# Optimization experiments

Hardware: AMD Instinct MI355X
Metric: run time of the kernel (lower is better)

Reference implementation:

```python
import jax, jax.numpy as jnp
import numpy as np

INFTY_APPROX = 1e30
LAM = 10000.0


def sinusoid_embs(length, width):
    # Transformer-XL sinusoidal embeddings, flipped so row 0 encodes the
    # largest relative distance (length-1), matching the rel_shift convention.
    pos = jnp.arange(length, dtype=jnp.float32)
    inv_lams = 1.0 / (LAM ** (jnp.arange(0, width, 2, dtype=jnp.float32) / width))
    pre = pos[:, None] * inv_lams[None, :]                 # [T, width//2]
    cat = jnp.concatenate([jnp.sin(pre), jnp.cos(pre)], axis=-1)  # [T, width]
    return jnp.flip(cat, axis=0)


def rel_shift(x):
    # x: [B, T, T] -> out[b,i,j] = x[b, i, j - i + T - 1] (XL pad/reshape trick)
    b, t, _ = x.shape
    x = jnp.pad(x, ((0, 0), (0, 0), (1, 0)))               # [B, T, T+1]
    x = x.reshape(b, t + 1, t)[:, 1:, :]                   # [B, T, T]
    return x


def setup_inputs() -> dict:
    B, T, D, K, V = 2, 4096, 1024, 128, 2048
    key = jax.random.key(0)
    ks = jax.random.split(key, 10)
    s_d = 1.0 / np.sqrt(D)
    s_v = 1.0 / np.sqrt(V)
    return {
        'x':    jax.random.normal(ks[0], (B, T, D), dtype=jnp.float32),
        'g_ln': jnp.ones((D,), dtype=jnp.float32),
        'W_q':  s_d * jax.random.normal(ks[1], (D, K), dtype=jnp.float32),
        'W_k':  s_d * jax.random.normal(ks[2], (D, K), dtype=jnp.float32),
        'W_v':  s_d * jax.random.normal(ks[3], (D, V), dtype=jnp.float32),
        'W_g':  s_d * jax.random.normal(ks[4], (D, V), dtype=jnp.float32),
        'W_r':  s_d * jax.random.normal(ks[5], (D, K), dtype=jnp.float32),
        'xl_u': 0.02 * jax.random.normal(ks[6], (K,), dtype=jnp.float32),
        'xl_v': 0.02 * jax.random.normal(ks[7], (K,), dtype=jnp.float32),
        'W_o':  s_v * jax.random.normal(ks[8], (V, D), dtype=jnp.float32),
    }


def reference(x, g_ln, W_q, W_k, W_v, W_g, W_r, xl_u, xl_v, W_o):
    B, T, D = x.shape
    K = W_q.shape[-1]
    tau = jnp.asarray(K, x.dtype) ** 0.5

    # RMSNorm input layernorm
    x_tilde = x * jax.lax.rsqrt(jnp.mean(jnp.square(x), axis=-1, keepdims=True) + 1e-6)
    x_tilde = x_tilde * g_ln

    # QKVG projections; queries pre-scaled by 1/tau (producer-side scaling)
    q = (x_tilde @ W_q) / tau                              # [B, T, K]
    k = x_tilde @ W_k                                      # [B, T, K]
    v = x_tilde @ W_v                                      # [B, T, V]

    # XL relative-position bias inputs
    xl_r = sinusoid_embs(T, D) @ W_r                       # [T, K]

    # AC term (content) and BD term (position) with XL u/v biases
    scores_ac = jnp.einsum('bik,bjk->bij', q + xl_u, k)    # [B, T, T]
    scores_bd = jnp.einsum('bik,jk->bij', q + xl_v, xl_r)  # [B, T, T]
    scores_bd = rel_shift(scores_bd)

    scores = scores_ac + scores_bd
    keep = jnp.tril(jnp.ones((T, T), dtype=bool))          # causal keep mask
    scores = scores - jnp.asarray(INFTY_APPROX, x.dtype) * jnp.logical_not(keep)

    w = jax.nn.softmax(scores, axis=-1)                    # [B, T, T]
    wv = jnp.einsum('bij,bjv->biv', w, v)                  # [B, T, V]

    # SHGA gating (GAU-style silu gate)
    wv = wv * jax.nn.silu(x_tilde @ W_g)

    res = wv @ W_o                                         # [B, T, D]
    return res
```

## Files before the change

kernel.cpp:

```cpp
#include <hip/hip_runtime.h>
#include <hip/hip_bf16.h>
#include <stdint.h>

typedef __attribute__((ext_vector_type(4))) float f32x4;
typedef __attribute__((ext_vector_type(8))) short s16x8;
typedef __attribute__((ext_vector_type(8))) unsigned short u16x8;
typedef __attribute__((ext_vector_type(4))) unsigned short u16x4;

static __device__ __forceinline__ float b2f(unsigned short u) {
  union { unsigned int i; float f; } v; v.i = ((unsigned int)u) << 16; return v.f;
}
static __device__ __forceinline__ unsigned short f2b(float f) {
  unsigned int x = __float_as_uint(f);
  return (unsigned short)((x + 0x7fffu + ((x >> 16) & 1u)) >> 16);
}

typedef __attribute__((address_space(1))) const void gconst_t;
typedef __attribute__((address_space(3))) void lds_t;
static __device__ __forceinline__ void gload_lds16(const void* g, void* l) {
  __builtin_amdgcn_global_load_lds((gconst_t*)g, (lds_t*)l, 16, 0, 0);
}

template<int N>
static __device__ __forceinline__ void vmwait() {
  asm volatile("s_waitcnt vmcnt(%0)" :: "n"(N) : "memory");
}
static __device__ __forceinline__ void barmid() {
  __builtin_amdgcn_sched_barrier(0);
  __builtin_amdgcn_s_barrier();
  asm volatile("s_waitcnt lgkmcnt(0)" ::: "memory");
  __builtin_amdgcn_sched_barrier(0);
}
static __device__ __forceinline__ void barend() {
  __builtin_amdgcn_sched_barrier(0);
  __builtin_amdgcn_s_barrier();
}

struct GemmP {
  const unsigned short* A; const unsigned short* B; void* C;
  long sA, sB, sC;
  int M, N, K, lda, ldb, ldc;
  int causal, kend_mode, swapxy;
  int gxs, gys, qchunk;
  const float* uvec; const float* vvec;
  unsigned short* qv_out; unsigned short* kk_out; float invtau;
  const float* rinv; const unsigned short* gate;
  const unsigned short* bds; float* stats;
};

template<int EPI>
__launch_bounds__(512, 2)
__global__ void gemm8p256_k(GemmP p) {
  __shared__ unsigned short L[2][4][8192];
  const int lin = (int)blockIdx.x + (int)gridDim.x * ((int)blockIdx.y + (int)gridDim.y * (int)blockIdx.z);
  const int wg = (lin & 7) * p.qchunk + (lin >> 3);
  const int xx = wg & ((1 << p.gxs) - 1);
  const int yy = (wg >> p.gxs) & ((1 << p.gys) - 1);
  const int ii = p.swapxy ? yy : xx;
  const int jj = p.swapxy ? xx : yy;
  const int i0 = ii * 256, j0 = jj * 256;
  const unsigned short* Ag = p.A + (long)i0 * p.lda;
  const unsigned short* Bg = p.B + (long)j0 * p.ldb;
  const int lda = p.lda, ldb = p.ldb;
  const int NI = p.K >> 7;

  const int tid = threadIdx.x;
  const int w = tid >> 6, l = tid & 63;
  const int wr = w >> 2, wc = w & 3;
  const int fr = l & 15, fq = l >> 4;

  auto stA = [&](int slot, int h, int t) {
#pragma unroll
    for (int u = 0; u < 2; ++u) {
      const int sl = u * 512 + tid, r = sl >> 3, g = sl & 7;
      const int gs = g ^ (r & 7);
      gload_lds16(Ag + (long)(h * 128 + r) * lda + t * 64 + gs * 8, &L[slot][h][sl * 8]);
    }
  };
  auto stB = [&](int slot, int h, int t) {
#pragma unroll
    for (int u = 0; u < 2; ++u) {
      const int sl = u * 512 + tid, r = sl >> 3, g = sl & 7;
      const int gs = g ^ (r & 7);
      gload_lds16(Bg + (long)(h * 128 + r) * ldb + t * 64 + gs * 8, &L[slot][2 + h][sl * 8]);
    }
  };

  f32x4 acc[8][4];
#pragma unroll
  for (int m = 0; m < 8; ++m)
#pragma unroll
    for (int n = 0; n < 4; ++n) acc[m][n] = (f32x4){0.f, 0.f, 0.f, 0.f};

  const int sx = (fr & 7) << 4;
  const int abase = ((fr << 7) + (fq << 4)) ^ sx;
  const int bbase = (((wc & 1) << 13) + (fr << 7) + (fq << 4)) ^ sx;
  s16x8 a[4][2], bA[2][2], bB[2][2];

  auto rdA = [&](int slot, int mq) {
#pragma unroll
    for (int m = 0; m < 4; ++m)
#pragma unroll
      for (int ks = 0; ks < 2; ++ks)
        a[m][ks] = *(const s16x8*)((const char*)&L[slot][wr][0] +
                                   ((abase ^ (ks << 6)) | ((mq * 4 + m) << 11)));
  };
  auto rdB = [&](int slot, int nq, s16x8 (&bb)[2][2]) {
    const int reg = 2 + (wc >> 1);
#pragma unroll
    for (int n = 0; n < 2; ++n)
#pragma unroll
      for (int ks = 0; ks < 2; ++ks)
        bb[n][ks] = *(const s16x8*)((const char*)&L[slot][reg][0] +
                                    ((bbase ^ (ks << 6)) | ((nq * 2 + n) << 11)));
  };
  auto mm = [&](int mq, int nq, s16x8 (&bb)[2][2]) {
    __builtin_amdgcn_s_setprio(1);
#pragma unroll
    for (int m = 0; m < 4; ++m)
#pragma unroll
      for (int n = 0; n < 2; ++n)
#pragma unroll
        for (int ks = 0; ks < 2; ++ks)
          acc[mq * 4 + m][nq * 2 + n] =
              __builtin_amdgcn_mfma_f32_16x16x32_bf16(a[m][ks], bb[n][ks],
                                                      acc[mq * 4 + m][nq * 2 + n], 0, 0, 0);
    __builtin_amdgcn_s_setprio(0);
  };

  stB(0, 0, 0); stB(0, 1, 0); stA(0, 0, 0); stA(0, 1, 0);
  stB(1, 0, 1); stB(1, 1, 1);
  vmwait<4>();
  barend();

  for (int it = 0; it < NI; ++it) {
    const int t0 = 2 * it, t1 = t0 + 1;
    const bool lastI = (it == NI - 1);
    rdA(0, 0); rdB(0, 0, bA); stA(1, 0, t1);
    barmid(); mm(0, 0, bA); barend();
    rdB(0, 1, bB); stA(1, 1, t1);
    barmid(); mm(0, 1, bB); barend();
    rdA(0, 1);
    if (!lastI) stB(0, 0, t0 + 2);
    barmid(); mm(1, 1, bB); barend();
    if (!lastI) stB(0, 1, t0 + 2);
    barmid(); mm(1, 0, bA);
    if (lastI) vmwait<0>(); else vmwait<4>();
    barend();
    rdA(1, 0); rdB(1, 0, bA);
    if (!lastI) stA(0, 0, t0 + 2);
    barmid(); mm(0, 0, bA); barend();
    rdB(1, 1, bB);
    if (!lastI) stA(0, 1, t0 + 2);
    barmid(); mm(0, 1, bB); barend();
    rdA(1, 1);
    if (!lastI) stB(1, 0, t1 + 2);
    barmid(); mm(1, 1, bB); barend();
    if (!lastI) stB(1, 1, t1 + 2);
    barmid(); mm(1, 0, bA);
    if (!lastI) vmwait<4>();
    barend();
  }

  const int rb = i0 + wr * 128 + fq * 4;
  const int cb = j0 + wc * 64 + fr;
#pragma unroll
  for (int m = 0; m < 8; ++m)
#pragma unroll
    for (int n = 0; n < 4; ++n) {
      const int col = cb + n * 16;
#pragma unroll
      for (int e = 0; e < 4; ++e) {
        const int row = rb + m * 16 + e;
        const float val = acc[m][n][e];
        if constexpr (EPI == 0)
          ((unsigned short*)p.C)[(long)row * p.ldc + col] = f2b(val);
        else
          ((unsigned short*)p.C)[(long)row * p.ldc + col] = f2b(val / (1.f + __expf(-val)));
      }
    }
}

template<int PAIR, int EPI>
__launch_bounds__(512, 2)
__global__ void gemm8p128_k(GemmP p) {
  __shared__ unsigned short L[3][3][8192];
  const int lin = (int)blockIdx.x + (int)gridDim.x * ((int)blockIdx.y + (int)gridDim.y * (int)blockIdx.z);
  const int wg = (lin & 7) * p.qchunk + (lin >> 3);
  const int xx = wg & ((1 << p.gxs) - 1);
  const int yy = (wg >> p.gxs) & ((1 << p.gys) - 1);
  const int b  = wg >> (p.gxs + p.gys);
  const int jj = PAIR ? yy : (p.swapxy ? xx : yy);
  const int j0 = jj * 128;
  const unsigned short* Bg0 = p.B + (long)b * p.sB + (long)j0 * p.ldb;
  const int lda = p.lda, ldb = p.ldb;

  const int tid = threadIdx.x;
  const int w = tid >> 6, l = tid & 63;
  const int wr = w >> 1, wc = w & 1;
  const int fr = l & 15, fq = l >> 4;

  const int sx = (fr & 7) << 4;
  const int abase = ((((wr & 1) << 13) + (fr << 7) + (fq << 4))) ^ sx;
  const int bbase = (((wc << 13) + (fr << 7) + (fq << 4))) ^ sx;

  const int passes = PAIR ? 2 : 1;
  for (int ps = 0; ps < passes; ++ps) {
    const int ii = PAIR ? (ps ? xx : (15 - xx)) : (p.swapxy ? yy : xx);
    const int i0 = ii * 256;
    const unsigned short* Ag = p.A + (long)b * p.sA + (long)i0 * lda;
    const int kend = p.kend_mode ? min(p.K, i0 + 256) : p.K;
    const int NT = kend >> 6;

    auto stA = [&](int slot, int h, int t) {
#pragma unroll
      for (int u = 0; u < 2; ++u) {
        const int sl = u * 512 + tid, r = sl >> 3, g = sl & 7;
        const int gs = g ^ (r & 7);
        gload_lds16(Ag + (long)(h * 128 + r) * lda + t * 64 + gs * 8, &L[slot][h][sl * 8]);
      }
    };
    auto stB = [&](int slot, int bh, int t) {
      const int r = tid >> 3, g = tid & 7;
      const int rloc = bh * 64 + r;
      const int gs = g ^ (rloc & 7);
      gload_lds16(Bg0 + (long)rloc * ldb + t * 64 + gs * 8, &L[slot][2][bh * 4096 + tid * 8]);
    };

    f32x4 acc[4][4];
#pragma unroll
    for (int m = 0; m < 4; ++m)
#pragma unroll
      for (int n = 0; n < 4; ++n) acc[m][n] = (f32x4){0.f, 0.f, 0.f, 0.f};
    s16x8 a[4][2], bA[2][2], bB[2][2];

    auto rdA = [&](int slot) {
      const int reg = wr >> 1;
#pragma unroll
      for (int m = 0; m < 4; ++m)
#pragma unroll
        for (int ks = 0; ks < 2; ++ks)
          a[m][ks] = *(const s16x8*)((const char*)&L[slot][reg][0] +
                                     ((abase ^ (ks << 6)) | (m << 11)));
    };
    auto rdB = [&](int slot, int nq, s16x8 (&bb)[2][2]) {
#pragma unroll
      for (int n = 0; n < 2; ++n)
#pragma unroll
        for (int ks = 0; ks < 2; ++ks)
          bb[n][ks] = *(const s16x8*)((const char*)&L[slot][2][0] +
                                      ((bbase ^ (ks << 6)) | ((nq * 2 + n) << 11)));
    };
    auto mm = [&](int nq, s16x8 (&bb)[2][2]) {
      __builtin_amdgcn_s_setprio(1);
#pragma unroll
      for (int m = 0; m < 4; ++m)
#pragma unroll
        for (int n = 0; n < 2; ++n)
#pragma unroll
          for (int ks = 0; ks < 2; ++ks)
            acc[m][nq * 2 + n] =
                __builtin_amdgcn_mfma_f32_16x16x32_bf16(a[m][ks], bb[n][ks],
                                                        acc[m][nq * 2 + n], 0, 0, 0);
      __builtin_amdgcn_s_setprio(0);
    };

    stA(0, 0, 0); stB(0, 0, 0); stA(0, 1, 0); stB(0, 1, 0);
    stA(1, 0, 1); stB(1, 0, 1); stA(1, 1, 1); stB(1, 1, 1);
    vmwait<6>();
    barend();

    int s = 0;
    for (int t = 0; t < NT; ++t) {
      int s2 = s + 2; if (s2 >= 3) s2 -= 3;
      const bool pf = (t + 2 < NT);
      rdA(s); rdB(s, 0, bA);
      if (pf) { stA(s2, 0, t + 2); stB(s2, 0, t + 2); }
      barmid(); mm(0, bA); barend();
      rdB(s, 1, bB);
      if (pf) { stA(s2, 1, t + 2); stB(s2, 1, t + 2); }
      barmid(); mm(1, bB);
      if (t == NT - 2) vmwait<0>(); else if (t < NT - 2) vmwait<6>();
      barend();
      s = (s + 1 == 3) ? 0 : s + 1;
    }

    const int rb = i0 + wr * 64 + fq * 4;
    const int cb = j0 + wc * 64 + fr;
    const long tb = (long)b * p.sC;
#pragma unroll
    for (int m = 0; m < 4; ++m)
#pragma unroll
      for (int n = 0; n < 4; ++n) {
        const int col = cb + n * 16;
#pragma unroll
        for (int e = 0; e < 4; ++e) {
          const int row = rb + m * 16 + e;
          const float val = acc[m][n][e];
          if constexpr (EPI == 1) {
            ((float*)p.C)[tb + (long)row * p.ldc + col] = val;
          } else {
            const long coff = tb + (long)row * p.ldc + col;
            const float g = b2f(p.gate[coff]);
            const float r = p.rinv[b * p.M + row];
            ((unsigned short*)p.C)[coff] = f2b(val * r * g);
          }
        }
      }
  }
}

template<int NREP, int EPI>
__launch_bounds__(512, 4)
__global__ void gemm2p_k(GemmP p) {
  constexpr int BN = NREP * 64;
  constexpr int CB = NREP / 2;
  constexpr int LPT = 1 + CB;
  const int lin = (int)blockIdx.x + (((int)blockIdx.y + (int)blockIdx.z * (int)gridDim.y) << p.gxs);
  const int wg = (lin & 7) * p.qchunk + (lin >> 3);
  const int ii = wg & ((1 << p.gxs) - 1);
  const int jj = (wg >> p.gxs) & ((1 << p.gys) - 1);
  const int b  = wg >> (p.gxs + p.gys);
  const int i0 = ii * 128, j0 = jj * BN;
  if (p.causal && j0 > i0 + 127) return;
  const unsigned short* Ag = p.A + (long)b * p.sA + (long)i0 * p.lda;
  const unsigned short* Bg = p.B + (long)b * p.sB + (long)j0 * p.ldb;
  const int NT = p.K >> 5;

  __shared__ unsigned short As[3][128 * 32];
  __shared__ unsigned short Bs[3][BN * 32];

  const int tid = threadIdx.x;
  const int w = tid >> 6, l = tid & 63;
  const int wr = w >> 2, wc = w & 3;
  const int lrow = l >> 2;
  const int swz = ((l & 3) ^ ((l >> 3) & 3)) * 8;

  auto stage = [&](int t, int bi) {
    gload_lds16(Ag + (long)(w * 16 + lrow) * p.lda + t * 32 + swz, &As[bi][w * 512]);
#pragma unroll
    for (int i = 0; i < CB; ++i) {
      const int c = w * CB + i;
      gload_lds16(Bg + (long)(c * 16 + lrow) * p.ldb + t * 32 + swz, &Bs[bi][c * 512]);
    }
  };

  f32x4 acc[4][NREP];
#pragma unroll
  for (int m = 0; m < 4; ++m)
#pragma unroll
    for (int n = 0; n < NREP; ++n) acc[m][n] = (f32x4){0.f, 0.f, 0.f, 0.f};

  const int fr = l & 15, fq = l >> 4;
  const int rg = (fq ^ ((fr >> 1) & 3)) * 8;
  const int aoff = (wr * 64 + fr) * 32 + rg;
  const int boff = (wc * (NREP * 16) + fr) * 32 + rg;

  stage(0, 0);
  if (NT > 1) stage(1, 1);

  int bi = 0;
  for (int t = 0; t < NT; ++t) {
    if (t == NT - 1) vmwait<0>(); else vmwait<LPT>();
    __builtin_amdgcn_s_barrier();
    __builtin_amdgcn_sched_barrier(0);
    const unsigned short* as = &As[bi][0];
    const unsigned short* bs = &Bs[bi][0];
    s16x8 af[4], bf[NREP];
#pragma unroll
    for (int m = 0; m < 4; ++m) af[m] = *(const s16x8*)(as + aoff + m * 512);
#pragma unroll
    for (int n = 0; n < NREP; ++n) bf[n] = *(const s16x8*)(bs + boff + n * 512);
    if (t + 2 < NT) {
      int bi2 = bi + 2; if (bi2 >= 3) bi2 -= 3;
      stage(t + 2, bi2);
    }
    __builtin_amdgcn_s_setprio(1);
#pragma unroll
    for (int m = 0; m < 4; ++m)
#pragma unroll
      for (int n = 0; n < NREP; ++n)
        acc[m][n] = __builtin_amdgcn_mfma_f32_16x16x32_bf16(af[m], bf[n], acc[m][n], 0, 0, 0);
    __builtin_amdgcn_s_setprio(0);
    bi = (bi + 1 == 3) ? 0 : bi + 1;
  }

  const int rbase = i0 + wr * 64 + fq * 4;
  const int cbase = j0 + wc * (NREP * 16) + fr;
  const long tb = (long)b * p.sC;

  if constexpr (EPI == 6) {
    float psum[16];
#pragma unroll
    for (int t = 0; t < 16; ++t) psum[t] = 0.f;
#pragma unroll
    for (int m = 0; m < 4; ++m)
#pragma unroll
      for (int n = 0; n < NREP; ++n) {
        const int col = cbase + n * 16;
#pragma unroll
        for (int e = 0; e < 4; ++e) {
          const int row = rbase + m * 16 + e;
          const long o = tb + (long)row * p.ldc + col;
          float ev = 0.f;
          if (col <= row) {
            const float s = acc[m][n][e] + b2f(p.bds[o]);
            ev = __expf(fminf(s, 60.f));
          }
          ((unsigned short*)p.C)[o] = f2b(ev);
          psum[m * 4 + e] += ev;
        }
      }
#pragma unroll
    for (int t = 0; t < 16; ++t) {
      float v = psum[t];
      v += __shfl_xor(v, 1); v += __shfl_xor(v, 2);
      v += __shfl_xor(v, 4); v += __shfl_xor(v, 8);
      psum[t] = v;
    }
    if (fr == 0) {
#pragma unroll
      for (int t = 0; t < 16; ++t) {
        const int row = rbase + (t >> 2) * 16 + (t & 3);
        p.stats[((long)(b * p.M + row) * 16 + jj) * 4 + wc] = psum[t];
      }
    }
    return;
  }

#pragma unroll
  for (int m = 0; m < 4; ++m)
#pragma unroll
    for (int n = 0; n < NREP; ++n) {
      const int col = cbase + n * 16;
#pragma unroll
      for (int e = 0; e < 4; ++e) {
        const int row = rbase + m * 16 + e;
        if constexpr (EPI == 5) {
          if (col <= row)
            ((unsigned short*)p.C)[tb + (long)row * p.ldc + (row - col)] = f2b(acc[m][n][e]);
        }
      }
    }
}

template<int EPI>
__launch_bounds__(256)
__global__ void gemm_bt_k(GemmP p) {
  const int i0 = blockIdx.x * 128;
  const int j0 = blockIdx.y * 128;
  const unsigned short* A = p.A + (long)i0 * p.lda;
  const unsigned short* B = p.B + (long)j0 * p.ldb;

  __shared__ unsigned short As[128 * 32];
  __shared__ unsigned short Bs[128 * 32];

  const int tid = threadIdx.x;
  const int w = tid >> 6, l = tid & 63;
  const int wr = w >> 1, wc = w & 1;

  f32x4 acc[4][4];
#pragma unroll
  for (int m = 0; m < 4; ++m)
#pragma unroll
    for (int n = 0; n < 4; ++n) acc[m][n] = (f32x4){0.f, 0.f, 0.f, 0.f};

  const int srow = (l >> 2);
  const int scol = ((l & 3) ^ ((l >> 3) & 3)) * 8;
  const unsigned short* ga0 = A + (long)(w * 16 + srow) * p.lda + scol;
  const unsigned short* ga1 = A + (long)((w + 4) * 16 + srow) * p.lda + scol;
  const unsigned short* gb0 = B + (long)(w * 16 + srow) * p.ldb + scol;
  const unsigned short* gb1 = B + (long)((w + 4) * 16 + srow) * p.ldb + scol;
  unsigned short* la0 = As + w * 512;
  unsigned short* la1 = As + (w + 4) * 512;
  unsigned short* lb0 = Bs + w * 512;
  unsigned short* lb1 = Bs + (w + 4) * 512;

  const int rg = ((l >> 4) ^ (((l & 15) >> 1) & 3)) * 8;
  const unsigned short* ap = As + ((wr * 64) + (l & 15)) * 32 + rg;
  const unsigned short* bp = Bs + ((wc * 64) + (l & 15)) * 32 + rg;

  for (int k0 = 0; k0 < p.K; k0 += 32) {
    gload_lds16(ga0 + k0, la0);
    gload_lds16(ga1 + k0, la1);
    gload_lds16(gb0 + k0, lb0);
    gload_lds16(gb1 + k0, lb1);
    __syncthreads();
    s16x8 af[4], bfr[4];
#pragma unroll
    for (int m = 0; m < 4; ++m) af[m] = *(const s16x8*)(ap + m * 16 * 32);
#pragma unroll
    for (int n = 0; n < 4; ++n) bfr[n] = *(const s16x8*)(bp + n * 16 * 32);
#pragma unroll
    for (int m = 0; m < 4; ++m)
#pragma unroll
      for (int n = 0; n < 4; ++n)
        acc[m][n] = __builtin_amdgcn_mfma_f32_16x16x32_bf16(af[m], bfr[n], acc[m][n], 0, 0, 0);
    __syncthreads();
  }

  const int rbase = i0 + wr * 64 + (l >> 4) * 4;
  const int cbase = j0 + wc * 64 + (l & 15);
#pragma unroll
  for (int m = 0; m < 4; ++m)
#pragma unroll
    for (int n = 0; n < 4; ++n) {
      const int col = cbase + n * 16;
#pragma unroll
      for (int e = 0; e < 4; ++e) {
        const int row = rbase + m * 16 + e;
        const float val = acc[m][n][e];
        if constexpr (EPI == 0) {
          ((unsigned short*)p.C)[(long)row * p.ldc + col] = f2b(val);
        } else if constexpr (EPI == 3) {
          if (j0 == 0) {
            const float q = val * p.invtau;
            const long o = (long)row * 128 + col;
            ((unsigned short*)p.C)[o] = f2b(q + p.uvec[col]);
            p.qv_out[o] = f2b(q + p.vvec[col]);
          } else {
            p.kk_out[(long)row * 128 + (col - 128)] = f2b(val);
          }
        }
      }
    }
}

__launch_bounds__(256)
__global__ void rmsnorm_k(const float* __restrict__ x, const float* __restrict__ g,
                          unsigned short* __restrict__ xt) {
  const long row = blockIdx.x;
  const float* xr = x + row * 1024;
  const int t = threadIdx.x;
  const float4 v = ((const float4*)xr)[t];
  float ss = v.x * v.x + v.y * v.y + v.z * v.z + v.w * v.w;
#pragma unroll
  for (int o = 1; o < 64; o <<= 1) ss += __shfl_xor(ss, o);
  __shared__ float wsum[4];
  if ((t & 63) == 0) wsum[t >> 6] = ss;
  __syncthreads();
  const float tot = wsum[0] + wsum[1] + wsum[2] + wsum[3];
  const float r = 1.0f / sqrtf(tot * (1.0f / 1024.0f) + 1e-6f);
  const float4 gv = ((const float4*)g)[t];
  u16x4 o;
  o.x = f2b(v.x * r * gv.x); o.y = f2b(v.y * r * gv.y);
  o.z = f2b(v.z * r * gv.z); o.w = f2b(v.w * r * gv.w);
  ((u16x4*)(xt + row * 1024))[t] = o;
}

__launch_bounds__(256)
__global__ void sinemb_k(unsigned short* __restrict__ emb) {
  const int idx = blockIdx.x * 256 + threadIdx.x;
  const int t = idx >> 10, w = idx & 1023;
  const int h = w & 511;
  const float inv = __expf(-(float)h * (9.2103403719761836f / 512.0f));
  const float pre = (float)t * inv;
  const float val = (w < 512) ? sinf(pre) : cosf(pre);
  emb[idx] = f2b(val);
}

struct TcP {
  const float* in[6];
  unsigned short* out[6];
  int R[6], C[6];
  int start[7];
};
__launch_bounds__(256)
__global__ void transcast6_k(TcP tc) {
  __shared__ float tile[32][33];
  const int bid = blockIdx.x;
  int m = 0;
#pragma unroll
  for (int i = 0; i < 6; ++i) if (bid >= tc.start[i + 1]) m = i + 1;
  const int local = bid - tc.start[m];
  const int R = tc.R[m], C = tc.C[m];
  const int tc_c = C >> 5;
  const int cx = local % tc_c, ry = local / tc_c;
  const int c0 = cx * 32, r0 = ry * 32;
  const float* in = tc.in[m];
  unsigned short* out = tc.out[m];
  const int tx = threadIdx.x & 31, ty = threadIdx.x >> 5;
#pragma unroll
  for (int k = 0; k < 4; ++k)
    tile[ty + k * 8][tx] = in[(long)(r0 + ty + k * 8) * C + c0 + tx];
  __syncthreads();
#pragma unroll
  for (int k = 0; k < 4; ++k)
    out[(long)(c0 + ty + k * 8) * R + r0 + tx] = f2b(tile[tx][ty + k * 8]);
}

__global__ void rowinv_k(const float* __restrict__ stats, float* __restrict__ rinv,
                         int T, int BT) {
  const int idx = blockIdx.x * 256 + threadIdx.x;
  if (idx >= BT) return;
  const int i = idx & (T - 1);
  const int nt = (i >> 8) + 1;
  const float* st = stats + (long)idx * 64;
  float s = 0.f;
  for (int jt = 0; jt < nt; ++jt)
    s += st[jt * 4] + st[jt * 4 + 1] + st[jt * 4 + 2] + st[jt * 4 + 3];
  rinv[idx] = 1.0f / s;
}

extern "C" void kernel_launch(void* const* d_in, const int* in_sizes, int n_in,
                              void* d_out, int out_size, void* d_ws, size_t ws_size,
                              hipStream_t stream) {
  const float* x    = (const float*)d_in[0];
  const float* g_ln = (const float*)d_in[1];
  const float* W_q  = (const float*)d_in[2];
  const float* W_k  = (const float*)d_in[3];
  const float* W_v  = (const float*)d_in[4];
  const float* W_g  = (const float*)d_in[5];
  const float* W_r  = (const float*)d_in[6];
  const float* xl_u = (const float*)d_in[7];
  const float* xl_v = (const float*)d_in[8];
  const float* W_o  = (const float*)d_in[9];
  float* out = (float*)d_out;

  const int B = 2, T = 4096, D = 1024, K = 128, V = 2048;
  const int BT = B * T;

  char* ws = (char*)d_ws;
  size_t off = 0;
  auto alloc = [&](size_t bytes) -> void* {
    void* p = ws + off; off += (bytes + 255) & ~(size_t)255; return p;
  };
  unsigned short* XT   = (unsigned short*)alloc((size_t)BT * D * 2);
  unsigned short* WQKT = (unsigned short*)alloc((size_t)256 * D * 2);
  unsigned short* WVT  = (unsigned short*)alloc((size_t)V * D * 2);
  unsigned short* WGT  = (unsigned short*)alloc((size_t)V * D * 2);
  unsigned short* WRT  = (unsigned short*)alloc((size_t)K * D * 2);
  unsigned short* WOT  = (unsigned short*)alloc((size_t)D * V * 2);
  unsigned short* QU   = (unsigned short*)alloc((size_t)BT * K * 2);
  unsigned short* QV   = (unsigned short*)alloc((size_t)BT * K * 2);
  unsigned short* KKb  = (unsigned short*)alloc((size_t)BT * K * 2);
  unsigned short* RR   = (unsigned short*)alloc((size_t)T * K * 2);
  unsigned short* VVT  = (unsigned short*)alloc((size_t)V * BT * 2);
  unsigned short* GATE = (unsigned short*)alloc((size_t)BT * V * 2);
  float* STATS         = (float*)alloc((size_t)BT * 64 * 4);
  float* RINV          = (float*)alloc((size_t)BT * 4);
  unsigned short* EBUF = (unsigned short*)alloc((size_t)B * T * T * 2);
  unsigned short* BD2  = (unsigned short*)alloc((size_t)B * T * T * 2);
  unsigned short* EMB  = BD2;
  unsigned short* WVG  = BD2;
  if (off > ws_size) return;
  (void)in_sizes; (void)n_in; (void)out_size;

  const float invtau = 0.08838834764831845f;

  {
    TcP tc{};
    const float* ins[6]  = {W_q, W_k, W_v, W_g, W_r, W_o};
    unsigned short* os[6] = {WQKT, WQKT + (size_t)K * D, WVT, WGT, WRT, WOT};
    const int Rs[6] = {D, D, D, D, D, V};
    const int Cs[6] = {K, K, V, V, K, D};
    int acc = 0;
    for (int i = 0; i < 6; ++i) {
      tc.in[i] = ins[i]; tc.out[i] = os[i]; tc.R[i] = Rs[i]; tc.C[i] = Cs[i];
      tc.start[i] = acc; acc += (Rs[i] / 32) * (Cs[i] / 32);
    }
    tc.start[6] = acc;
    transcast6_k<<<acc, 256, 0, stream>>>(tc);
  }
  rmsnorm_k<<<BT, 256, 0, stream>>>(x, g_ln, XT);
  sinemb_k<<<(T * D) / 256, 256, 0, stream>>>(EMB);

  {
    GemmP p{}; p.A = XT; p.B = WQKT; p.C = QU;
    p.M = BT; p.N = 256; p.K = D; p.lda = D; p.ldb = D; p.ldc = K;
    p.uvec = xl_u; p.vvec = xl_v; p.qv_out = QV; p.kk_out = KKb; p.invtau = invtau;
    gemm_bt_k<3><<<dim3(BT / 128, 2, 1), 256, 0, stream>>>(p);
  }
  {
    GemmP p{}; p.A = EMB; p.B = WRT; p.C = RR;
    p.M = T; p.N = K; p.K = D; p.lda = D; p.ldb = D; p.ldc = K;
    gemm_bt_k<0><<<dim3(T / 128, 1, 1), 256, 0, stream>>>(p);
  }
  {
    GemmP p{}; p.A = WVT; p.B = XT; p.C = VVT;
    p.M = V; p.N = BT; p.K = D; p.lda = D; p.ldb = D; p.ldc = BT;
    p.gxs = 3; p.gys = 5; p.qchunk = 32; p.swapxy = 0;
    gemm8p256_k<0><<<dim3(8, 32, 1), 512, 0, stream>>>(p);
  }
  {
    GemmP p{}; p.A = XT; p.B = WGT; p.C = GATE;
    p.M = BT; p.N = V; p.K = D; p.lda = D; p.ldb = D; p.ldc = V;
    p.gxs = 3; p.gys = 5; p.qchunk = 32; p.swapxy = 1;
    gemm8p256_k<2><<<dim3(8, 32, 1), 512, 0, stream>>>(p);
  }
  {
    GemmP p{}; p.A = QV; p.B = RR; p.C = BD2;
    p.sA = (long)T * K; p.sB = 0; p.sC = (long)T * T;
    p.M = T; p.N = T; p.K = K; p.lda = K; p.ldb = K; p.ldc = T; p.causal = 1;
    p.gxs = 5; p.gys = 4; p.qchunk = 128;
    gemm2p_k<4, 5><<<dim3(32, 16, B), 512, 0, stream>>>(p);
  }
  {
    GemmP p{}; p.A = QU; p.B = KKb; p.C = EBUF;
    p.sA = (long)T * K; p.sB = (long)T * K; p.sC = (long)T * T;
    p.M = T; p.N = T; p.K = K; p.lda = K; p.ldb = K; p.ldc = T; p.causal = 1;
    p.bds = BD2; p.stats = STATS;
    p.gxs = 5; p.gys = 4; p.qchunk = 128;
    gemm2p_k<4, 6><<<dim3(32, 16, B), 512, 0, stream>>>(p);
  }
  rowinv_k<<<BT / 256, 256, 0, stream>>>(STATS, RINV, T, BT);
  {
    GemmP p{}; p.A = EBUF; p.B = VVT; p.C = WVG;
    p.sA = (long)T * T; p.sB = T; p.sC = (long)T * V;
    p.M = T; p.N = V; p.K = T; p.lda = T; p.ldb = BT; p.ldc = V;
    p.kend_mode = 1; p.rinv = RINV; p.gate = GATE;
    p.gxs = 3; p.gys = 4; p.qchunk = 32;
    gemm8p128_k<1, 4><<<dim3(8, 16, 2), 512, 0, stream>>>(p);
  }
  {
    GemmP p{}; p.A = WVG; p.B = WOT; p.C = out;
    p.M = BT; p.N = D; p.K = V; p.lda = V; p.ldb = V; p.ldc = D;
    p.gxs = 3; p.gys = 5; p.qchunk = 32; p.swapxy = 1;
    gemm8p128_k<0, 1><<<dim3(8, 32, 1), 512, 0, stream>>>(p);
  }
}
```

Measured before the change: 398.4 us.

## Fuse positional BD score GEMM into content score kernel via LDS rel-shift

Replaces the two-kernel scheme, which wrote the full rel-shifted BD scores to a B*T*T bf16 buffer and then read them back in the AC/exp kernel, with one kernel per 128x128 tile. Each tile computes the needed 128x256 band of Q_v·R^T into LDS, computes Q_u·K^T, and gathers the shifted BD value from LDS when forming exp scores and row partial sums. This removes a large global write and read of the T*T BD matrix. In exchange it recomputes twice the BD work per tile, uses much more LDS (lowering occupancy), and shrinks tiles to 128 wide, which doubles the stats entries.

```diff
diff --git a/kernel.cpp b/kernel.cpp
--- a/kernel.cpp
+++ b/kernel.cpp
@@ -45,7 +45,6 @@
   const float* uvec; const float* vvec;
   unsigned short* qv_out; unsigned short* kk_out; float invtau;
   const float* rinv; const unsigned short* gate;
-  const unsigned short* bds; float* stats;
 };
 
 template<int EPI>
@@ -310,138 +309,181 @@
   }
 }
 
-template<int NREP, int EPI>
-__launch_bounds__(512, 4)
-__global__ void gemm2p_k(GemmP p) {
-  constexpr int BN = NREP * 64;
-  constexpr int CB = NREP / 2;
-  constexpr int LPT = 1 + CB;
-  const int lin = (int)blockIdx.x + (((int)blockIdx.y + (int)blockIdx.z * (int)gridDim.y) << p.gxs);
+struct EsP {
+  const unsigned short *QU, *QV, *KK, *RR;
+  unsigned short* E; float* stats;
+  int T, qchunk;
+};
+__launch_bounds__(512)
+__global__ void escore_k(EsP p) {
+  __shared__ unsigned short As[3][128 * 32];
+  __shared__ unsigned short Bs[3][256 * 32];
+  __shared__ unsigned short BDl[128 * 256];
+  const int T = p.T;
+  const int lin = (int)blockIdx.x + (int)gridDim.x * ((int)blockIdx.y + (int)gridDim.y * (int)blockIdx.z);
   const int wg = (lin & 7) * p.qchunk + (lin >> 3);
-  const int ii = wg & ((1 << p.gxs) - 1);
-  const int jj = (wg >> p.gxs) & ((1 << p.gys) - 1);
-  const int b  = wg >> (p.gxs + p.gys);
-  const int i0 = ii * 128, j0 = jj * BN;
-  if (p.causal && j0 > i0 + 127) return;
-  const unsigned short* Ag = p.A + (long)b * p.sA + (long)i0 * p.lda;
-  const unsigned short* Bg = p.B + (long)b * p.sB + (long)j0 * p.ldb;
-  const int NT = p.K >> 5;
-
-  __shared__ unsigned short As[3][128 * 32];
-  __shared__ unsigned short Bs[3][BN * 32];
-
+  const int ii = wg & 31;
+  const int jj = (wg >> 5) & 31;
+  const int b  = wg >> 10;
+  const int i0 = ii * 128, j0 = jj * 128;
+  const long tb = (long)b * T * T;
   const int tid = threadIdx.x;
+
+  if (j0 > i0 + 127) {
+    if (j0 == i0 + 128) {
+      const int r = tid >> 2, c = (tid & 3) * 32;
+      u16x8 z = (u16x8){0, 0, 0, 0, 0, 0, 0, 0};
+      u16x8* dst = (u16x8*)(p.E + tb + (long)(i0 + r) * T + j0 + c);
+      dst[0] = z; dst[1] = z; dst[2] = z; dst[3] = z;
+    }
+    return;
+  }
+
   const int w = tid >> 6, l = tid & 63;
   const int wr = w >> 2, wc = w & 3;
-  const int lrow = l >> 2;
-  const int swz = ((l & 3) ^ ((l >> 3) & 3)) * 8;
-
-  auto stage = [&](int t, int bi) {
-    gload_lds16(Ag + (long)(w * 16 + lrow) * p.lda + t * 32 + swz, &As[bi][w * 512]);
-#pragma unroll
-    for (int i = 0; i < CB; ++i) {
-      const int c = w * CB + i;
-      gload_lds16(Bg + (long)(c * 16 + lrow) * p.ldb + t * 32 + swz, &Bs[bi][c * 512]);
-    }
-  };
-
-  f32x4 acc[4][NREP];
-#pragma unroll
-  for (int m = 0; m < 4; ++m)
-#pragma unroll
-    for (int n = 0; n < NREP; ++n) acc[m][n] = (f32x4){0.f, 0.f, 0.f, 0.f};
-
   const int fr = l & 15, fq = l >> 4;
   const int rg = (fq ^ ((fr >> 1) & 3)) * 8;
-  const int aoff = (wr * 64 + fr) * 32 + rg;
-  const int boff = (wc * (NREP * 16) + fr) * 32 + rg;
-
-  stage(0, 0);
-  if (NT > 1) stage(1, 1);
-
-  int bi = 0;
-  for (int t = 0; t < NT; ++t) {
-    if (t == NT - 1) vmwait<0>(); else vmwait<LPT>();
-    __builtin_amdgcn_s_barrier();
-    __builtin_amdgcn_sched_barrier(0);
-    const unsigned short* as = &As[bi][0];
-    const unsigned short* bs = &Bs[bi][0];
-    s16x8 af[4], bf[NREP];
-#pragma unroll
-    for (int m = 0; m < 4; ++m) af[m] = *(const s16x8*)(as + aoff + m * 512);
-#pragma unroll
-    for (int n = 0; n < NREP; ++n) bf[n] = *(const s16x8*)(bs + boff + n * 512);
-    if (t + 2 < NT) {
-      int bi2 = bi + 2; if (bi2 >= 3) bi2 -= 3;
-      stage(t + 2, bi2);
-    }
-    __builtin_amdgcn_s_setprio(1);
+
+  const int dbase = max(0, i0 - j0 - 128);
+  const unsigned short* Aq = p.QV + (long)(b * T + i0) * 128;
+  const unsigned short* Br = p.RR + (long)dbase * 128;
+
+  auto stA = [&](const unsigned short* base, int t, int s) {
+    const int r = tid >> 2, g = tid & 3;
+    const int gs = g ^ ((r >> 1) & 3);
+    gload_lds16(base + (long)r * 128 + t * 32 + gs * 8, &As[s][tid * 8]);
+  };
+  auto stB256 = [&](const unsigned short* base, int t, int s) {
+#pragma unroll
+    for (int u = 0; u < 2; ++u) {
+      const int sl = u * 512 + tid, r = sl >> 2, g = sl & 3;
+      const int gs = g ^ ((r >> 1) & 3);
+      gload_lds16(base + (long)r * 128 + t * 32 + gs * 8, &Bs[s][sl * 8]);
+    }
+  };
+  auto stB128 = [&](const unsigned short* base, int t, int s) {
+    const int r = tid >> 2, g = tid & 3;
+    const int gs = g ^ ((r >> 1) & 3);
+    gload_lds16(base + (long)r * 128 + t * 32 + gs * 8, &Bs[s][tid * 8]);
+  };
+
+  {
+    f32x4 ac2[4][4];
 #pragma unroll
     for (int m = 0; m < 4; ++m)
 #pragma unroll
-      for (int n = 0; n < NREP; ++n)
-        acc[m][n] = __builtin_amdgcn_mfma_f32_16x16x32_bf16(af[m], bf[n], acc[m][n], 0, 0, 0);
-    __builtin_amdgcn_s_setprio(0);
-    bi = (bi + 1 == 3) ? 0 : bi + 1;
-  }
-
-  const int rbase = i0 + wr * 64 + fq * 4;
-  const int cbase = j0 + wc * (NREP * 16) + fr;
-  const long tb = (long)b * p.sC;
-
-  if constexpr (EPI == 6) {
-    float psum[16];
-#pragma unroll
-    for (int t = 0; t < 16; ++t) psum[t] = 0.f;
+      for (int n = 0; n < 4; ++n) ac2[m][n] = (f32x4){0.f, 0.f, 0.f, 0.f};
+    const int aoff = (wr * 64 + fr) * 32 + rg;
+    const int boff = (wc * 64 + fr) * 32 + rg;
+    stA(Aq, 0, 0); stB256(Br, 0, 0);
+    stA(Aq, 1, 1); stB256(Br, 1, 1);
+    int s = 0;
+    for (int t = 0; t < 4; ++t) {
+      if (t == 3) vmwait<0>(); else vmwait<3>();
+      __builtin_amdgcn_s_barrier();
+      __builtin_amdgcn_sched_barrier(0);
+      s16x8 af[4], bf[4];
+#pragma unroll
+      for (int m = 0; m < 4; ++m) af[m] = *(const s16x8*)(&As[s][0] + aoff + m * 512);
+#pragma unroll
+      for (int n = 0; n < 4; ++n) bf[n] = *(const s16x8*)(&Bs[s][0] + boff + n * 512);
+      if (t + 2 < 4) {
+        int s2 = s + 2; if (s2 >= 3) s2 -= 3;
+        stA(Aq, t + 2, s2); stB256(Br, t + 2, s2);
+      }
+      __builtin_amdgcn_s_setprio(1);
+#pragma unroll
+      for (int m = 0; m < 4; ++m)
+#pragma unroll
+        for (int n = 0; n < 4; ++n)
+          ac2[m][n] = __builtin_amdgcn_mfma_f32_16x16x32_bf16(af[m], bf[n], ac2[m][n], 0, 0, 0);
+      __builtin_amdgcn_s_setprio(0);
+      s = (s + 1 == 3) ? 0 : s + 1;
+    }
 #pragma unroll
     for (int m = 0; m < 4; ++m)
 #pragma unroll
-      for (int n = 0; n < NREP; ++n) {
-        const int col = cbase + n * 16;
+      for (int n = 0; n < 4; ++n)
 #pragma unroll
         for (int e = 0; e < 4; ++e) {
-          const int row = rbase + m * 16 + e;
-          const long o = tb + (long)row * p.ldc + col;
-          float ev = 0.f;
-          if (col <= row) {
-            const float s = acc[m][n][e] + b2f(p.bds[o]);
-            ev = __expf(fminf(s, 60.f));
-          }
-          ((unsigned short*)p.C)[o] = f2b(ev);
-          psum[m * 4 + e] += ev;
+          const int rl = wr * 64 + m * 16 + fq * 4 + e;
+          const int dc = wc * 64 + n * 16 + fr;
+          BDl[rl * 256 + dc] = f2b(ac2[m][n][e]);
         }
+  }
+  __syncthreads();
+
+  const unsigned short* Au = p.QU + (long)(b * T + i0) * 128;
+  const unsigned short* Bk = p.KK + (long)(b * T + j0) * 128;
+  f32x4 ac[4][2];
+#pragma unroll
+  for (int m = 0; m < 4; ++m)
+#pragma unroll
+    for (int n = 0; n < 2; ++n) ac[m][n] = (f32x4){0.f, 0.f, 0.f, 0.f};
+  {
+    const int aoff = (wr * 64 + fr) * 32 + rg;
+    const int boff = (wc * 32 + fr) * 32 + rg;
+    stA(Au, 0, 0); stB128(Bk, 0, 0);
+    stA(Au, 1, 1); stB128(Bk, 1, 1);
+    int s = 0;
+    for (int t = 0; t < 4; ++t) {
+      if (t == 3) vmwait<0>(); else vmwait<2>();
+      __builtin_amdgcn_s_barrier();
+      __builtin_amdgcn_sched_barrier(0);
+      s16x8 af[4], bf[2];
+#pragma unroll
+      for (int m = 0; m < 4; ++m) af[m] = *(const s16x8*)(&As[s][0] + aoff + m * 512);
+#pragma unroll
+      for (int n = 0; n < 2; ++n) bf[n] = *(const s16x8*)(&Bs[s][0] + boff + n * 512);
+      if (t + 2 < 4) {
+        int s2 = s + 2; if (s2 >= 3) s2 -= 3;
+        stA(Au, t + 2, s2); stB128(Bk, t + 2, s2);
       }
+      __builtin_amdgcn_s_setprio(1);
+#pragma unroll
+      for (int m = 0; m < 4; ++m)
+#pragma unroll
+        for (int n = 0; n < 2; ++n)
+          ac[m][n] = __builtin_amdgcn_mfma_f32_16x16x32_bf16(af[m], bf[n], ac[m][n], 0, 0, 0);
+      __builtin_amdgcn_s_setprio(0);
+      s = (s + 1 == 3) ? 0 : s + 1;
+    }
+  }
+
+  float psum[16];
+#pragma unroll
+  for (int t = 0; t < 16; ++t) psum[t] = 0.f;
+#pragma unroll
+  for (int m = 0; m < 4; ++m)
+#pragma unroll
+    for (int n = 0; n < 2; ++n)
+#pragma unroll
+      for (int e = 0; e < 4; ++e) {
+        const int rl = wr * 64 + m * 16 + fq * 4 + e;
+        const int cl = wc * 32 + n * 16 + fr;
+        const int d = (i0 + rl) - (j0 + cl);
+        float ev = 0.f;
+        if (d >= 0) {
+          const float sv = ac[m][n][e] + b2f(BDl[rl * 256 + (d - dbase)]);
+          ev = __expf(fminf(sv, 60.f));
+        }
+        p.E[tb + (long)(i0 + rl) * T + j0 + cl] = f2b(ev);
+        psum[m * 4 + e] += ev;
+      }
+#pragma unroll
+  for (int t = 0; t < 16; ++t) {
+    float v = psum[t];
+    v += __shfl_xor(v, 1); v += __shfl_xor(v, 2);
+    v += __shfl_xor(v, 4); v += __shfl_xor(v, 8);
+    psum[t] = v;
+  }
+  if (fr == 0) {
 #pragma unroll
     for (int t = 0; t < 16; ++t) {
-      float v = psum[t];
-      v += __shfl_xor(v, 1); v += __shfl_xor(v, 2);
-      v += __shfl_xor(v, 4); v += __shfl_xor(v, 8);
-      psum[t] = v;
-    }
-    if (fr == 0) {
-#pragma unroll
-      for (int t = 0; t < 16; ++t) {
-        const int row = rbase + (t >> 2) * 16 + (t & 3);
-        p.stats[((long)(b * p.M + row) * 16 + jj) * 4 + wc] = psum[t];
-      }
-    }
-    return;
-  }
-
-#pragma unroll
-  for (int m = 0; m < 4; ++m)
-#pragma unroll
-    for (int n = 0; n < NREP; ++n) {
-      const int col = cbase + n * 16;
-#pragma unroll
-      for (int e = 0; e < 4; ++e) {
-        const int row = rbase + m * 16 + e;
-        if constexpr (EPI == 5) {
-          if (col <= row)
-            ((unsigned short*)p.C)[tb + (long)row * p.ldc + (row - col)] = f2b(acc[m][n][e]);
-        }
-      }
-    }
+      const int row = i0 + wr * 64 + (t >> 2) * 16 + fq * 4 + (t & 3);
+      p.stats[((long)(b * T + row) * 32 + jj) * 4 + wc] = psum[t];
+    }
+  }
 }
 
 template<int EPI>
@@ -594,8 +636,8 @@
   const int idx = blockIdx.x * 256 + threadIdx.x;
   if (idx >= BT) return;
   const int i = idx & (T - 1);
-  const int nt = (i >> 8) + 1;
-  const float* st = stats + (long)idx * 64;
+  const int nt = (i >> 7) + 1;
+  const float* st = stats + (long)idx * 128;
   float s = 0.f;
   for (int jt = 0; jt < nt; ++jt)
     s += st[jt * 4] + st[jt * 4 + 1] + st[jt * 4 + 2] + st[jt * 4 + 3];
@@ -637,12 +679,11 @@
   unsigned short* RR   = (unsigned short*)alloc((size_t)T * K * 2);
   unsigned short* VVT  = (unsigned short*)alloc((size_t)V * BT * 2);
   unsigned short* GATE = (unsigned short*)alloc((size_t)BT * V * 2);
-  float* STATS         = (float*)alloc((size_t)BT * 64 * 4);
+  float* STATS         = (float*)alloc((size_t)BT * 128 * 4);
   float* RINV          = (float*)alloc((size_t)BT * 4);
   unsigned short* EBUF = (unsigned short*)alloc((size_t)B * T * T * 2);
-  unsigned short* BD2  = (unsigned short*)alloc((size_t)B * T * T * 2);
-  unsigned short* EMB  = BD2;
-  unsigned short* WVG  = BD2;
+  unsigned short* EMB  = (unsigned short*)alloc((size_t)T * D * 2);
+  unsigned short* WVG  = (unsigned short*)alloc((size_t)BT * V * 2);
   if (off > ws_size) return;
   (void)in_sizes; (void)n_in; (void)out_size;
 
@@ -689,19 +730,10 @@
     gemm8p256_k<2><<<dim3(8, 32, 1), 512, 0, stream>>>(p);
   }
   {
-    GemmP p{}; p.A = QV; p.B = RR; p.C = BD2;
-    p.sA = (long)T * K; p.sB = 0; p.sC = (long)T * T;
-    p.M = T; p.N = T; p.K = K; p.lda = K; p.ldb = K; p.ldc = T; p.causal = 1;
-    p.gxs = 5; p.gys = 4; p.qchunk = 128;
-    gemm2p_k<4, 5><<<dim3(32, 16, B), 512, 0, stream>>>(p);
-  }
-  {
-    GemmP p{}; p.A = QU; p.B = KKb; p.C = EBUF;
-    p.sA = (long)T * K; p.sB = (long)T * K; p.sC = (long)T * T;
-    p.M = T; p.N = T; p.K = K; p.lda = K; p.ldb = K; p.ldc = T; p.causal = 1;
-    p.bds = BD2; p.stats = STATS;
-    p.gxs = 5; p.gys = 4; p.qchunk = 128;
-    gemm2p_k<4, 6><<<dim3(32, 16, B), 512, 0, stream>>>(p);
+    EsP p{};
+    p.QU = QU; p.QV = QV; p.KK = KKb; p.RR = RR;
+    p.E = EBUF; p.stats = STATS; p.T = T; p.qchunk = 256;
+    escore_k<<<dim3(32, 32, 2), 512, 0, stream>>>(p);
   }
   rowinv_k<<<BT / 256, 256, 0, stream>>>(STATS, RINV, T, BT);
   {
```

Result: no change. 405.4 us (+1.8%).

## Run attention-weighted V GEMM on 256x256 tiles with causal k-limit and gated epilogue

Applied to the files above, without the earlier changes.

The P·V GEMM moves from the 128-wide paired kernel to the 256x256 tile kernel. That kernel gains batch strides, a causal k-end bound, a reversed row order so the longest causal tiles start first, and an epilogue that applies row-inverse normalization and the silu gate. Larger tiles raise arithmetic intensity per tile and cut reloads of A and B. The cost is coarser causal granularity (256-row blocks), more wasted work near the diagonal, and fewer workgroups (256).

```diff
diff --git a/kernel.cpp b/kernel.cpp
--- a/kernel.cpp
+++ b/kernel.cpp
@@ -56,13 +56,16 @@
   const int wg = (lin & 7) * p.qchunk + (lin >> 3);
   const int xx = wg & ((1 << p.gxs) - 1);
   const int yy = (wg >> p.gxs) & ((1 << p.gys) - 1);
-  const int ii = p.swapxy ? yy : xx;
+  const int b  = wg >> (p.gxs + p.gys);
+  int ii = p.swapxy ? yy : xx;
   const int jj = p.swapxy ? xx : yy;
+  if (p.kend_mode) ii = (1 << (p.swapxy ? p.gys : p.gxs)) - 1 - ii;
   const int i0 = ii * 256, j0 = jj * 256;
-  const unsigned short* Ag = p.A + (long)i0 * p.lda;
-  const unsigned short* Bg = p.B + (long)j0 * p.ldb;
+  const unsigned short* Ag = p.A + (long)b * p.sA + (long)i0 * p.lda;
+  const unsigned short* Bg = p.B + (long)b * p.sB + (long)j0 * p.ldb;
   const int lda = p.lda, ldb = p.ldb;
-  const int NI = p.K >> 7;
+  const int kend = p.kend_mode ? min(p.K, i0 + 256) : p.K;
+  const int NI = kend >> 7;
 
   const int tid = threadIdx.x;
   const int w = tid >> 6, l = tid & 63;
@@ -164,6 +167,7 @@
 
   const int rb = i0 + wr * 128 + fq * 4;
   const int cb = j0 + wc * 64 + fr;
+  const long tb = (long)b * p.sC;
 #pragma unroll
   for (int m = 0; m < 8; ++m)
 #pragma unroll
@@ -173,10 +177,17 @@
       for (int e = 0; e < 4; ++e) {
         const int row = rb + m * 16 + e;
         const float val = acc[m][n][e];
-        if constexpr (EPI == 0)
-          ((unsigned short*)p.C)[(long)row * p.ldc + col] = f2b(val);
-        else
-          ((unsigned short*)p.C)[(long)row * p.ldc + col] = f2b(val / (1.f + __expf(-val)));
+        if constexpr (EPI == 0) {
+          ((unsigned short*)p.C)[tb + (long)row * p.ldc + col] = f2b(val);
+        } else if constexpr (EPI == 2) {
+          ((unsigned short*)p.C)[tb + (long)row * p.ldc + col] =
+              f2b(val / (1.f + __expf(-val)));
+        } else {
+          const long coff = tb + (long)row * p.ldc + col;
+          const float g = b2f(p.gate[coff]);
+          const float r = p.rinv[b * p.M + row];
+          ((unsigned short*)p.C)[coff] = f2b(val * r * g);
+        }
       }
     }
 }
@@ -709,8 +720,8 @@
     p.sA = (long)T * T; p.sB = T; p.sC = (long)T * V;
     p.M = T; p.N = V; p.K = T; p.lda = T; p.ldb = BT; p.ldc = V;
     p.kend_mode = 1; p.rinv = RINV; p.gate = GATE;
-    p.gxs = 3; p.gys = 4; p.qchunk = 32;
-    gemm8p128_k<1, 4><<<dim3(8, 16, 2), 512, 0, stream>>>(p);
+    p.gxs = 4; p.gys = 3; p.qchunk = 32; p.swapxy = 0;
+    gemm8p256_k<4><<<dim3(16, 8, 2), 512, 0, stream>>>(p);
   }
   {
     GemmP p{}; p.A = WVG; p.B = WOT; p.C = out;
```

After: 431.2 us. 8.2% more time.
